# Kernel tuning notes

Measured on AMD Instinct MI355X. Metric: run time of the kernel, lower is better.

The kernel has to match this reference:

```python
import jax, jax.numpy as jnp
import numpy as np

B, T, I, H, O = 128, 512, 512, 2048, 512  # batch, seq_length, input, hidden, output


def setup_inputs() -> dict:
    key = jax.random.key(0)
    ks = jax.random.split(key, 8)
    s_ih = 1.0 / np.sqrt(H)  # torch RNNCell/Linear default init scale 1/sqrt(hidden)
    body = jax.random.normal(ks[0], (B, T - 1, I), dtype=jnp.float32)
    # last timestep row stores the integer pad index (as float), per the module's protocol
    pad = jax.random.randint(ks[1], (B,), 0, T - 2)
    last = jnp.broadcast_to(pad[:, None, None].astype(jnp.float32), (B, 1, I))
    x = jnp.concatenate([body, last], axis=1)  # [B, T, I]
    W_ih = jax.random.uniform(ks[2], (H, I), jnp.float32, -s_ih, s_ih)
    W_hh = jax.random.uniform(ks[3], (H, H), jnp.float32, -s_ih, s_ih)
    b_ih = jax.random.uniform(ks[4], (H,), jnp.float32, -s_ih, s_ih)
    b_hh = jax.random.uniform(ks[5], (H,), jnp.float32, -s_ih, s_ih)
    W_fc = jax.random.uniform(ks[6], (O, H), jnp.float32, -s_ih, s_ih)
    b_fc = jax.random.uniform(ks[7], (O,), jnp.float32, -s_ih, s_ih)
    h0 = jnp.ones((H,), jnp.float32)  # self.h parameter, ones-initialized
    return {"x": x, "h0": h0, "W_ih": W_ih, "b_ih": b_ih, "W_hh": W_hh,
            "b_hh": b_hh, "W_fc": W_fc, "b_fc": b_fc}


def reference(x, h0, W_ih, b_ih, W_hh, b_hh, W_fc, b_fc):
    steps = T - 2  # loop runs over x.shape[2]-1 = (T-1)-1 timesteps
    pad = x[:, -1, 0].astype(jnp.int32)          # [B] pad indices
    xs = jnp.transpose(x[:, :steps, :], (1, 0, 2))  # [steps, B, I]
    h_init = jnp.broadcast_to(h0, (x.shape[0], H))  # self.h * ones([B,1])

    def step(h, xt):
        h = jnp.tanh(xt @ W_ih.T + b_ih + h @ W_hh.T + b_hh)
        return h, h @ W_fc.T + b_fc

    _, outs = jax.lax.scan(step, h_init, xs)     # [steps, B, O]
    # mask selects the single timestep j == pad_len[b]; everything else is zeroed
    mask = (pad[None, :] == jnp.arange(steps)[:, None]).astype(outs.dtype)  # [steps, B]
    return jnp.sum(outs * mask[:, :, None], axis=0)  # [B, O]
```

## Files before the change

kernel.cpp:

```cpp
#include <hip/hip_runtime.h>

#define Bsz 128
#define Tsz 512
#define Isz 512
#define Hsz 2048
#define Osz 512
#define STEPS 510

typedef short short8 __attribute__((ext_vector_type(8)));
typedef float floatx4 __attribute__((ext_vector_type(4)));

__device__ __forceinline__ unsigned short f2bf(float f) {
  unsigned int u = __builtin_bit_cast(unsigned int, f);
  u += 0x7FFFu + ((u >> 16) & 1u);
  return (unsigned short)(u >> 16);
}

template <int AUX>
__device__ __forceinline__ void gload_lds16(const void* g, void* l) {
  __builtin_amdgcn_global_load_lds(
      (const __attribute__((address_space(1))) void*)g,
      (__attribute__((address_space(3))) void*)l, 16, 0, AUX);
}

__global__ __launch_bounds__(256, 1)
void rnn_kernel(const float* __restrict__ x, const float* __restrict__ h0v,
                const float* __restrict__ W_ih, const float* __restrict__ b_ih,
                const float* __restrict__ W_hh, const float* __restrict__ b_hh,
                unsigned short* __restrict__ hbuf,
                float* __restrict__ hfinal,
                unsigned int* __restrict__ flags)
{
  __shared__ short h_lds[4 * 8192];
  __shared__ float red_lds[4 * 1024];
  __shared__ int pad_lds[16];

  const int tid = threadIdx.x;
  const int lane = tid & 63;
  const int wv = tid >> 6;
  const int m16 = lane & 15;
  const int quad = lane >> 4;
  const int m7 = m16 & 7;
  const int rg = blockIdx.x & 7;
  const int cg = blockIdx.x >> 3;
  const int b0 = rg * 16;
  const int c0 = cg * 64;
  const int kq = wv * 512;
  const int kqx = wv * 128;
  const int wvoff = wv * 8192;

  short8 wf[16][4];
  short8 wih[4][4];
#pragma unroll
  for (int nt = 0; nt < 4; ++nt) {
    const int wrow = c0 + nt * 16 + m16;
    const float* base = W_hh + (size_t)wrow * Hsz + kq + quad * 8;
#pragma unroll
    for (int kc = 0; kc < 16; ++kc) {
      short8 v;
#pragma unroll
      for (int j = 0; j < 8; ++j) v[j] = (short)f2bf(base[kc * 32 + j]);
      wf[kc][nt] = v;
    }
    const float* basex = W_ih + (size_t)wrow * Isz + kqx + quad * 8;
#pragma unroll
    for (int kc = 0; kc < 4; ++kc) {
      short8 v;
#pragma unroll
      for (int j = 0; j < 8; ++j) v[j] = (short)f2bf(basex[kc * 32 + j]);
      wih[kc][nt] = v;
    }
  }

  const int rrow = tid >> 4;
  const int rcb = (tid & 15) * 4;
  float bias[4];
#pragma unroll
  for (int i = 0; i < 4; ++i) bias[i] = b_ih[c0 + rcb + i] + b_hh[c0 + rcb + i];

  if (tid < 16)
    pad_lds[tid] = (int)x[(size_t)(b0 + tid) * (Tsz * Isz) + (size_t)(Tsz - 1) * Isz];

  for (int i = lane; i < 1024; i += 64) {
    const int c = i >> 7;
    const int r = (i >> 3) & 15;
    const int u = i & 7;
    const int k = kq + c * 64 + u * 8;
    short8 v;
#pragma unroll
    for (int j = 0; j < 8; ++j) v[j] = (short)f2bf(h0v[k + j]);
    *reinterpret_cast<short8*>(&h_lds[wvoff + c * 1024 + r * 64 + (u ^ (r & 7)) * 8]) = v;
  }

  const unsigned int* fp = flags + (size_t)(wv * 8 + (lane & 7)) * 8 + rg;

  for (int t = 0; t < STEPS; ++t) {
    const bool have_next = (t + 1) < STEPS;

    const float* xp = x + (size_t)(b0 + m16) * (Tsz * Isz) + (size_t)t * Isz + kqx + quad * 8;
    float4 xv[8];
#pragma unroll
    for (int kcc = 0; kcc < 4; ++kcc) {
      xv[2 * kcc] = *reinterpret_cast<const float4*>(xp + kcc * 32);
      xv[2 * kcc + 1] = *reinterpret_cast<const float4*>(xp + kcc * 32 + 4);
    }

    if (t > 0) {
      while (!__all((int)(__hip_atomic_load(fp, __ATOMIC_RELAXED,
                                            __HIP_MEMORY_SCOPE_AGENT) >= (unsigned)t)))
        __builtin_amdgcn_s_sleep(1);
      const unsigned short* hsrcp = hbuf + (size_t)(t & 1) * (Bsz * Hsz);
#pragma unroll
      for (int c = 0; c < 8; ++c) {
        const unsigned short* src = hsrcp + (size_t)((wv * 8 + c) * 8 + rg) * 1024;
        gload_lds16<0x11>(src + lane * 8, &h_lds[wvoff + c * 1024]);
        gload_lds16<0x11>(src + 512 + lane * 8, &h_lds[wvoff + c * 1024 + 512]);
      }
    }

    short8 xa[4];
#pragma unroll
    for (int kcc = 0; kcc < 4; ++kcc) {
      short8 a;
      a[0] = (short)f2bf(xv[2 * kcc].x);
      a[1] = (short)f2bf(xv[2 * kcc].y);
      a[2] = (short)f2bf(xv[2 * kcc].z);
      a[3] = (short)f2bf(xv[2 * kcc].w);
      a[4] = (short)f2bf(xv[2 * kcc + 1].x);
      a[5] = (short)f2bf(xv[2 * kcc + 1].y);
      a[6] = (short)f2bf(xv[2 * kcc + 1].z);
      a[7] = (short)f2bf(xv[2 * kcc + 1].w);
      xa[kcc] = a;
    }

    floatx4 acc[4];
#pragma unroll
    for (int nt = 0; nt < 4; ++nt) {
      floatx4 zero = {0.f, 0.f, 0.f, 0.f};
      acc[nt] = zero;
    }
#pragma unroll
    for (int kcc = 0; kcc < 4; ++kcc)
#pragma unroll
      for (int nt = 0; nt < 4; ++nt)
        acc[nt] = __builtin_amdgcn_mfma_f32_16x16x32_bf16(xa[kcc], wih[kcc][nt], acc[nt], 0, 0, 0);

    __builtin_amdgcn_s_waitcnt(0x0F78);
#pragma unroll
    for (int c = 0; c < 4; ++c) {
      const int base = wvoff + c * 1024 + m16 * 64;
#pragma unroll
      for (int k2 = 0; k2 < 2; ++k2) {
        const short8 a =
            *reinterpret_cast<const short8*>(&h_lds[base + ((k2 * 4 + quad) ^ m7) * 8]);
#pragma unroll
        for (int nt = 0; nt < 4; ++nt)
          acc[nt] = __builtin_amdgcn_mfma_f32_16x16x32_bf16(a, wf[c * 2 + k2][nt], acc[nt], 0, 0, 0);
      }
    }
    __builtin_amdgcn_s_waitcnt(0x0F70);
#pragma unroll
    for (int c = 4; c < 8; ++c) {
      const int base = wvoff + c * 1024 + m16 * 64;
#pragma unroll
      for (int k2 = 0; k2 < 2; ++k2) {
        const short8 a =
            *reinterpret_cast<const short8*>(&h_lds[base + ((k2 * 4 + quad) ^ m7) * 8]);
#pragma unroll
        for (int nt = 0; nt < 4; ++nt)
          acc[nt] = __builtin_amdgcn_mfma_f32_16x16x32_bf16(a, wf[c * 2 + k2][nt], acc[nt], 0, 0, 0);
      }
    }

#pragma unroll
    for (int nt = 0; nt < 4; ++nt)
#pragma unroll
      for (int i = 0; i < 4; ++i)
        red_lds[wv * 1024 + (quad * 4 + i) * 64 + nt * 16 + m16] = acc[nt][i];

    __syncthreads();

    {
      float4 z = {0.f, 0.f, 0.f, 0.f};
#pragma unroll
      for (int ww = 0; ww < 4; ++ww) {
        const float4 p =
            *reinterpret_cast<const float4*>(&red_lds[ww * 1024 + rrow * 64 + rcb]);
        z.x += p.x; z.y += p.y; z.z += p.z; z.w += p.w;
      }
      const float t0 = tanhf(z.x + bias[0]);
      const float t1 = tanhf(z.y + bias[1]);
      const float t2 = tanhf(z.z + bias[2]);
      const float t3 = tanhf(z.w + bias[3]);
      unsigned long long pk = (unsigned long long)f2bf(t0) |
                              ((unsigned long long)f2bf(t1) << 16) |
                              ((unsigned long long)f2bf(t2) << 32) |
                              ((unsigned long long)f2bf(t3) << 48);
      const int toff = rrow * 64 + ((rcb >> 3) ^ (rrow & 7)) * 8 + ((rcb >> 2) & 1) * 4;
      unsigned short* hd = hbuf + (size_t)((t + 1) & 1) * (Bsz * Hsz) +
                           (size_t)(cg * 8 + rg) * 1024 + toff;
      __hip_atomic_store(reinterpret_cast<unsigned long long*>(hd), pk,
                         __ATOMIC_RELAXED, __HIP_MEMORY_SCOPE_AGENT);
      if (pad_lds[rrow] == t) {
        float4 o;
        o.x = t0; o.y = t1; o.z = t2; o.w = t3;
        *reinterpret_cast<float4*>(&hfinal[(size_t)(b0 + rrow) * Hsz + c0 + rcb]) = o;
      }
    }

    __syncthreads();

    if (have_next && tid == 0) {
      __hip_atomic_store(flags + cg * 8 + rg, (unsigned)(t + 1),
                         __ATOMIC_RELAXED, __HIP_MEMORY_SCOPE_AGENT);
    }
  }
}

__global__ __launch_bounds__(64)
void fc_kernel(const float* __restrict__ hfinal, const float* __restrict__ W_fc,
               const float* __restrict__ b_fc, float* __restrict__ out) {
  const int lane = threadIdx.x & 63;
  const int m16 = lane & 15;
  const int quad = lane >> 4;
  const int b0 = (blockIdx.x & 7) * 16;
  const int o0 = (blockIdx.x >> 3) * 16;
  floatx4 acc = {0.f, 0.f, 0.f, 0.f};
  const float* ap = hfinal + (size_t)(b0 + m16) * Hsz + quad * 8;
  const float* bp = W_fc + (size_t)(o0 + m16) * Hsz + quad * 8;
#pragma unroll 4
  for (int kc = 0; kc < 64; ++kc) {
    short8 a, b;
#pragma unroll
    for (int j = 0; j < 8; ++j) a[j] = (short)f2bf(ap[kc * 32 + j]);
#pragma unroll
    for (int j = 0; j < 8; ++j) b[j] = (short)f2bf(bp[kc * 32 + j]);
    acc = __builtin_amdgcn_mfma_f32_16x16x32_bf16(a, b, acc, 0, 0, 0);
  }
  const float bias = b_fc[o0 + m16];
#pragma unroll
  for (int i = 0; i < 4; ++i)
    out[(size_t)(b0 + quad * 4 + i) * Osz + o0 + m16] = acc[i] + bias;
}

__global__ void zero_flags(unsigned int* f) { f[threadIdx.x] = 0u; }

extern "C" void kernel_launch(void* const* d_in, const int* in_sizes, int n_in,
                              void* d_out, int out_size, void* d_ws, size_t ws_size,
                              hipStream_t stream) {
  const float* x = (const float*)d_in[0];
  const float* h0 = (const float*)d_in[1];
  const float* W_ih = (const float*)d_in[2];
  const float* b_ih = (const float*)d_in[3];
  const float* W_hh = (const float*)d_in[4];
  const float* b_hh = (const float*)d_in[5];
  const float* W_fc = (const float*)d_in[6];
  const float* b_fc = (const float*)d_in[7];
  float* out = (float*)d_out;

  char* ws = (char*)d_ws;
  unsigned short* hbuf = (unsigned short*)ws;
  float* hfinal = (float*)(ws + (1u << 20));
  unsigned int* flags = (unsigned int*)(ws + (2u << 20));

  zero_flags<<<1, 256, 0, stream>>>(flags);
  rnn_kernel<<<256, 256, 0, stream>>>(x, h0, W_ih, b_ih, W_hh, b_hh, hbuf, hfinal, flags);
  fc_kernel<<<256, 64, 0, stream>>>(hfinal, W_fc, b_fc, out);
}
```

Baseline: 2.277 ms.

## Detect same-XCC block groups to use L2-coherent hidden-state exchange; fast tanh

At kernel start, each block records its XCC id into a shared array. Each row group of blocks then checks whether all of its blocks sit on the same XCC. If they do, hidden-state exchange uses plain stores and cached loads instead of system-coherent (nontemporal/SC-bit) loads and atomic stores, which is meant to cut the cross-step latency of the serial recurrence. It also replaces tanhf with an exp/rcp approximation to shorten the per-step epilogue. The risks are extra startup spinning on the XCC array and relying on L2 coherence, which only holds within one XCC.

```diff
diff --git a/kernel.cpp b/kernel.cpp
--- a/kernel.cpp
+++ b/kernel.cpp
@@ -16,6 +16,11 @@
   return (unsigned short)(u >> 16);
 }
 
+__device__ __forceinline__ float tanh_fast(float x) {
+  const float e = __expf(2.f * x);
+  return 1.f - 2.f * __builtin_amdgcn_rcpf(e + 1.f);
+}
+
 template <int AUX>
 __device__ __forceinline__ void gload_lds16(const void* g, void* l) {
   __builtin_amdgcn_global_load_lds(
@@ -29,11 +34,13 @@
                 const float* __restrict__ W_hh, const float* __restrict__ b_hh,
                 unsigned short* __restrict__ hbuf,
                 float* __restrict__ hfinal,
-                unsigned int* __restrict__ flags)
+                unsigned int* __restrict__ flags,
+                unsigned int* __restrict__ xcc_arr)
 {
   __shared__ short h_lds[4 * 8192];
   __shared__ float red_lds[4 * 1024];
   __shared__ int pad_lds[16];
+  __shared__ unsigned int mode_lds;
 
   const int tid = threadIdx.x;
   const int lane = tid & 63;
@@ -49,6 +56,25 @@
   const int kqx = wv * 128;
   const int wvoff = wv * 8192;
 
+  {
+    unsigned int xcc;
+    asm volatile("s_getreg_b32 %0, hwreg(HW_REG_XCC_ID)" : "=s"(xcc));
+    if (tid == 0)
+      __hip_atomic_store(&xcc_arr[rg * 32 + cg], xcc + 1u, __ATOMIC_RELAXED,
+                         __HIP_MEMORY_SCOPE_AGENT);
+    if (wv == 0) {
+      const unsigned int* ap = &xcc_arr[rg * 32 + (lane & 31)];
+      unsigned int v;
+      do {
+        v = __hip_atomic_load(ap, __ATOMIC_RELAXED, __HIP_MEMORY_SCOPE_AGENT);
+        if (__all((int)(v != 0u))) break;
+        __builtin_amdgcn_s_sleep(2);
+      } while (true);
+      const int same = __all((int)(v == xcc + 1u));
+      if (tid == 0) mode_lds = (unsigned int)same;
+    }
+  }
+
   short8 wf[16][4];
   short8 wih[4][4];
 #pragma unroll
@@ -92,6 +118,9 @@
     *reinterpret_cast<short8*>(&h_lds[wvoff + c * 1024 + r * 64 + (u ^ (r & 7)) * 8]) = v;
   }
 
+  __syncthreads();
+  const bool use_l2 = (mode_lds != 0u);
+
   const unsigned int* fp = flags + (size_t)(wv * 8 + (lane & 7)) * 8 + rg;
 
   for (int t = 0; t < STEPS; ++t) {
@@ -110,11 +139,20 @@
                                             __HIP_MEMORY_SCOPE_AGENT) >= (unsigned)t)))
         __builtin_amdgcn_s_sleep(1);
       const unsigned short* hsrcp = hbuf + (size_t)(t & 1) * (Bsz * Hsz);
-#pragma unroll
-      for (int c = 0; c < 8; ++c) {
-        const unsigned short* src = hsrcp + (size_t)((wv * 8 + c) * 8 + rg) * 1024;
-        gload_lds16<0x11>(src + lane * 8, &h_lds[wvoff + c * 1024]);
-        gload_lds16<0x11>(src + 512 + lane * 8, &h_lds[wvoff + c * 1024 + 512]);
+      if (use_l2) {
+#pragma unroll
+        for (int c = 0; c < 8; ++c) {
+          const unsigned short* src = hsrcp + (size_t)((wv * 8 + c) * 8 + rg) * 1024;
+          gload_lds16<0x01>(src + lane * 8, &h_lds[wvoff + c * 1024]);
+          gload_lds16<0x01>(src + 512 + lane * 8, &h_lds[wvoff + c * 1024 + 512]);
+        }
+      } else {
+#pragma unroll
+        for (int c = 0; c < 8; ++c) {
+          const unsigned short* src = hsrcp + (size_t)((wv * 8 + c) * 8 + rg) * 1024;
+          gload_lds16<0x11>(src + lane * 8, &h_lds[wvoff + c * 1024]);
+          gload_lds16<0x11>(src + 512 + lane * 8, &h_lds[wvoff + c * 1024 + 512]);
+        }
       }
     }
 
@@ -188,10 +226,10 @@
             *reinterpret_cast<const float4*>(&red_lds[ww * 1024 + rrow * 64 + rcb]);
         z.x += p.x; z.y += p.y; z.z += p.z; z.w += p.w;
       }
-      const float t0 = tanhf(z.x + bias[0]);
-      const float t1 = tanhf(z.y + bias[1]);
-      const float t2 = tanhf(z.z + bias[2]);
-      const float t3 = tanhf(z.w + bias[3]);
+      const float t0 = tanh_fast(z.x + bias[0]);
+      const float t1 = tanh_fast(z.y + bias[1]);
+      const float t2 = tanh_fast(z.z + bias[2]);
+      const float t3 = tanh_fast(z.w + bias[3]);
       unsigned long long pk = (unsigned long long)f2bf(t0) |
                               ((unsigned long long)f2bf(t1) << 16) |
                               ((unsigned long long)f2bf(t2) << 32) |
@@ -199,8 +237,12 @@
       const int toff = rrow * 64 + ((rcb >> 3) ^ (rrow & 7)) * 8 + ((rcb >> 2) & 1) * 4;
       unsigned short* hd = hbuf + (size_t)((t + 1) & 1) * (Bsz * Hsz) +
                            (size_t)(cg * 8 + rg) * 1024 + toff;
-      __hip_atomic_store(reinterpret_cast<unsigned long long*>(hd), pk,
-                         __ATOMIC_RELAXED, __HIP_MEMORY_SCOPE_AGENT);
+      if (use_l2) {
+        *reinterpret_cast<unsigned long long*>(hd) = pk;
+      } else {
+        __hip_atomic_store(reinterpret_cast<unsigned long long*>(hd), pk,
+                           __ATOMIC_RELAXED, __HIP_MEMORY_SCOPE_AGENT);
+      }
       if (pad_lds[rrow] == t) {
         float4 o;
         o.x = t0; o.y = t1; o.z = t2; o.w = t3;
@@ -243,7 +285,7 @@
     out[(size_t)(b0 + quad * 4 + i) * Osz + o0 + m16] = acc[i] + bias;
 }
 
-__global__ void zero_flags(unsigned int* f) { f[threadIdx.x] = 0u; }
+__global__ void zero_flags(unsigned int* f) { f[blockIdx.x * 256 + threadIdx.x] = 0u; }
 
 extern "C" void kernel_launch(void* const* d_in, const int* in_sizes, int n_in,
                               void* d_out, int out_size, void* d_ws, size_t ws_size,
@@ -262,8 +304,10 @@
   unsigned short* hbuf = (unsigned short*)ws;
   float* hfinal = (float*)(ws + (1u << 20));
   unsigned int* flags = (unsigned int*)(ws + (2u << 20));
-
-  zero_flags<<<1, 256, 0, stream>>>(flags);
-  rnn_kernel<<<256, 256, 0, stream>>>(x, h0, W_ih, b_ih, W_hh, b_hh, hbuf, hfinal, flags);
+  unsigned int* xcc_arr = flags + 256;
+
+  zero_flags<<<2, 256, 0, stream>>>(flags);
+  rnn_kernel<<<256, 256, 0, stream>>>(x, h0, W_ih, b_ih, W_hh, b_hh, hbuf, hfinal,
+                                      flags, xcc_arr);
   fc_kernel<<<256, 64, 0, stream>>>(hfinal, W_fc, b_fc, out);
 }
```

Result: faster. 2.070 ms (-9.1%).
